# Optimization experiments

Measured on AMD Instinct MI355X. Metric: run time of the kernel, lower is better.

Reference implementation:

```python
import jax, jax.numpy as jnp
import numpy as np

# Static config matching init_kwargs
DG = 8          # deformable groups
KH, KW = 3, 3
STRIDE, PAD, DIL = 1, 1, 1


def setup_inputs() -> dict:
    key = jax.random.key(0)
    k1, k2, k3, k4 = jax.random.split(key, 4)
    B, C, H, W = 4, 128, 128, 128
    Cout = 128
    K = KH * KW
    x = jax.random.normal(k1, (B, C, H, W), dtype=jnp.float32)
    offset = jax.random.normal(k2, (B, 2 * DG * K, H, W), dtype=jnp.float32)
    mask = jax.random.uniform(k3, (B, DG * K, H, W), dtype=jnp.float32)
    stdv = 1.0 / np.sqrt(C * KH * KW)
    weight = jax.random.uniform(k4, (Cout, C, KH, KW), dtype=jnp.float32,
                                minval=-stdv, maxval=stdv)
    bias = jnp.zeros((Cout,), dtype=jnp.float32)
    return {"x": x, "offset": offset, "mask": mask, "weight": weight, "bias": bias}


def _deform_conv2d(x, offset, mask, weight, bias):
    B, C, H, W = x.shape
    Cout = weight.shape[0]
    K = KH * KW
    Ho = (H + 2 * PAD - DIL * (KH - 1) - 1) // STRIDE + 1
    Wo = (W + 2 * PAD - DIL * (KW - 1) - 1) // STRIDE + 1
    Cg = C // DG

    # offsets: channel layout [dg, k, (dy, dx)]
    off = offset.reshape(B, DG, K, 2, Ho, Wo)
    dy, dx = off[:, :, :, 0], off[:, :, :, 1]          # [B, DG, K, Ho, Wo]
    m = mask.reshape(B, DG, K, Ho, Wo)

    ky, kx = jnp.meshgrid(jnp.arange(KH), jnp.arange(KW), indexing='ij')
    ky, kx = ky.reshape(K), kx.reshape(K)
    # base sampling grid per kernel tap: [K, Ho] / [K, Wo]
    py = (jnp.arange(Ho) * STRIDE - PAD)[None, :] + (ky * DIL)[:, None]
    px = (jnp.arange(Wo) * STRIDE - PAD)[None, :] + (kx * DIL)[:, None]

    sy = dy + py[None, None, :, :, None].astype(dy.dtype)  # [B, DG, K, Ho, Wo]
    sx = dx + px[None, None, :, None, :].astype(dx.dtype)

    y0f = jnp.floor(sy); x0f = jnp.floor(sx)
    ly = sy - y0f; lx = sx - x0f
    y0 = y0f.astype(jnp.int32); x0 = x0f.astype(jnp.int32)

    x_g = x.reshape(B, DG, Cg, H * W)

    def gather(iy, ix):
        valid = ((iy >= 0) & (iy < H) & (ix >= 0) & (ix < W)).astype(x.dtype)
        idx = jnp.clip(iy, 0, H - 1) * W + jnp.clip(ix, 0, W - 1)
        flat = idx.reshape(B, DG, 1, K * Ho * Wo)
        v = jnp.take_along_axis(x_g, flat, axis=3).reshape(B, DG, Cg, K, Ho, Wo)
        return v * valid[:, :, None]

    w00 = ((1 - ly) * (1 - lx))[:, :, None]
    w01 = ((1 - ly) * lx)[:, :, None]
    w10 = (ly * (1 - lx))[:, :, None]
    w11 = (ly * lx)[:, :, None]

    val = (gather(y0, x0) * w00 + gather(y0, x0 + 1) * w01 +
           gather(y0 + 1, x0) * w10 + gather(y0 + 1, x0 + 1) * w11)
    val = val * m[:, :, None]                         # modulation
    sampled = val.reshape(B, C, K, Ho, Wo)

    w = weight.reshape(Cout, C, K)
    out = jnp.einsum('bckhw,ock->bohw', sampled, w)
    return out + bias[None, :, None, None]


def reference(x, offset, mask, weight, bias):
    return _deform_conv2d(x, offset, mask, weight, bias)
```

## Files before the change

kernel.cpp:

```cpp
#include <hip/hip_runtime.h>
#include <hip/hip_fp16.h>


#define NB    4
#define NC    128
#define NH    128
#define NW    128
#define NCOUT 128
#define NDG   8
#define NCG   16
#define NK    9
#define NCK   1152
#define NHW   16384
#define GK    160
#define ROWP  168
#define WROW  1280

typedef __attribute__((ext_vector_type(4))) float f32x4;
typedef _Float16 half8 __attribute__((ext_vector_type(8)));

union C16 { uint4 u[2]; __half2 h[8]; };

__device__ __forceinline__ unsigned pk2h(float a, float b) {
  return (unsigned)__half_as_ushort(__float2half_rn(a)) |
         ((unsigned)__half_as_ushort(__float2half_rn(b)) << 16);
}

__global__ __launch_bounds__(256)
void prep(const float* __restrict__ x, const float* __restrict__ w,
          ushort* __restrict__ xt, ushort* __restrict__ wf) {
  __shared__ __align__(16) unsigned LDSU[1024 * 9];
  const int tid = threadIdx.x;

  if (blockIdx.x < 128) {
    const int o = blockIdx.x;
    float* WL = (float*)LDSU;
    const float4* src = (const float4*)(w + o * NCK);
    for (int i = tid; i < NCK / 4; i += 256) ((float4*)WL)[i] = src[i];
    __syncthreads();
    unsigned* dst = (unsigned*)wf + o * (WROW / 2);
    for (int t = tid; t < WROW / 2; t += 256) {
      const int g = t / 80, r = t - g * 80;
      unsigned v = 0;
      if (r < 72) {
        const int k = r >> 3;
        const int c = g * NCG + (r & 7) * 2;
        v = pk2h(WL[c * NK + k], WL[(c + 1) * NK + k]);
      }
      dst[t] = v;
    }
  } else {
    const int blk  = blockIdx.x - 128;
    const int slab = blk >> 4;
    const int hw0  = (blk & 15) * 1024;
    const float* xb = x + (size_t)slab * NCG * NHW + hw0;
#pragma unroll
    for (int cp = 0; cp < 8; ++cp) {
#pragma unroll
      for (int i = 0; i < 4; ++i) {
        const int hw = tid + 256 * i;
        LDSU[hw * 9 + cp] =
            pk2h(xb[(2 * cp) * NHW + hw], xb[(2 * cp + 1) * NHW + hw]);
      }
    }
    __syncthreads();
    uint4* dst = (uint4*)(xt + ((size_t)slab * NHW + hw0) * NCG);
#pragma unroll
    for (int j = 0; j < 8; ++j) {
      const int lin = tid + 256 * j;
      const int hw = lin >> 1, q = lin & 1;
      uint4 v;
      v.x = LDSU[hw * 9 + q * 4 + 0];
      v.y = LDSU[hw * 9 + q * 4 + 1];
      v.z = LDSU[hw * 9 + q * 4 + 2];
      v.w = LDSU[hw * 9 + q * 4 + 3];
      dst[lin] = v;
    }
  }
}

__device__ __forceinline__ void sample_one(
    int p, int k, int g, int b, int ho, int wo0,
    float dy, float dx, float mm,
    const ushort* __restrict__ xt, ushort* __restrict__ S) {
  const int ky = k / 3, kx = k - ky * 3;

  const float sy = dy + (float)(ho - 1 + ky);
  const float sx = dx + (float)(wo0 + p - 1 + kx);
  const float y0f = floorf(sy), x0f = floorf(sx);
  const float ly = sy - y0f, lx = sx - x0f;
  const int y0 = (int)y0f, x0 = (int)x0f;
  const int y1 = y0 + 1,  x1 = x0 + 1;
  const float hy = 1.f - ly, hx = 1.f - lx;

  float w00 = hy * hx * mm, w01 = hy * lx * mm;
  float w10 = ly * hx * mm, w11 = ly * lx * mm;
  if (y0 < 0 || y0 >= NH) { w00 = 0.f; w01 = 0.f; }
  if (y1 < 0 || y1 >= NH) { w10 = 0.f; w11 = 0.f; }
  if (x0 < 0 || x0 >= NW) { w00 = 0.f; w10 = 0.f; }
  if (x1 < 0 || x1 >= NW) { w01 = 0.f; w11 = 0.f; }

  const int yc0 = min(max(y0, 0), NH - 1);
  const int yc1 = min(max(y1, 0), NH - 1);
  const int xc0 = min(max(x0, 0), NW - 1);
  const int xc1 = min(max(x1, 0), NW - 1);

  const ushort* xg = xt + (size_t)(b * NDG + g) * NHW * NCG;
  const uint4* q00 = (const uint4*)(xg + (yc0 * NW + xc0) * NCG);
  const uint4* q01 = (const uint4*)(xg + (yc0 * NW + xc1) * NCG);
  const uint4* q10 = (const uint4*)(xg + (yc1 * NW + xc0) * NCG);
  const uint4* q11 = (const uint4*)(xg + (yc1 * NW + xc1) * NCG);

  C16 v00, v01, v10, v11, r;
  v00.u[0] = q00[0]; v00.u[1] = q00[1];
  v01.u[0] = q01[0]; v01.u[1] = q01[1];
  v10.u[0] = q10[0]; v10.u[1] = q10[1];
  v11.u[0] = q11[0]; v11.u[1] = q11[1];

  const __half2 W00 = __float2half2_rn(w00);
  const __half2 W01 = __float2half2_rn(w01);
  const __half2 W10 = __float2half2_rn(w10);
  const __half2 W11 = __float2half2_rn(w11);
#pragma unroll
  for (int i = 0; i < 8; ++i) {
    __half2 a = __hmul2(v00.h[i], W00);
    a = __hfma2(v01.h[i], W01, a);
    a = __hfma2(v10.h[i], W10, a);
    a = __hfma2(v11.h[i], W11, a);
    r.h[i] = a;
  }
  ushort* dp = &S[p * ROWP + k * 16];
  *(uint4*)dp = r.u[0];
  *((uint4*)dp + 1) = r.u[1];
}

__global__ __launch_bounds__(256, 4)
void dcn_main(const float* __restrict__ off,
              const float* __restrict__ msk,
              const ushort* __restrict__ xt,
              const ushort* __restrict__ wf,
              const float* __restrict__ bias,
              float* __restrict__ out) {
  __shared__ __align__(16) ushort S[64 * ROWP];

  const int tid  = threadIdx.x;
  const int blk0 = blockIdx.x;
  const int blk  = (blk0 & 7) * 128 + (blk0 >> 3);
  const int b    = blk >> 8;
  const int ho   = (blk >> 1) & 127;
  const int wo0  = (blk & 1) * 64;

  const int lane = tid & 63;
  const int wv   = tid >> 6;
  const int l15  = lane & 15;
  const int kq   = lane >> 4;

  const float* offB = off + (size_t)b * 144 * NHW + ho * NW + wo0;
  const float* mskB = msk + (size_t)b * 72  * NHW + ho * NW + wo0;

  for (int i = tid; i < 64 * 8; i += 256) {
    ((unsigned*)S)[(i >> 3) * (ROWP / 2) + 72 + (i & 7)] = 0;
  }

  f32x4 acc[4][2];
#pragma unroll
  for (int m = 0; m < 4; ++m) {
    acc[m][0] = {0.f, 0.f, 0.f, 0.f};
    acc[m][1] = {0.f, 0.f, 0.f, 0.f};
  }

  const int p0 = tid & 63;
  const int k0 = tid >> 6;
  const int k1 = k0 + 4;

  float dy0, dx0, mm0, dy1, dx1, mm1, dy2 = 0.f, dx2 = 0.f, mm2 = 0.f;
  {
    const int gka = k0, gkb = k1;
    dy0 = offB[(gka * 2) * NHW + p0];
    dx0 = offB[(gka * 2 + 1) * NHW + p0];
    mm0 = mskB[gka * NHW + p0];
    dy1 = offB[(gkb * 2) * NHW + p0];
    dx1 = offB[(gkb * 2 + 1) * NHW + p0];
    mm1 = mskB[gkb * NHW + p0];
    if (tid < 64) {
      dy2 = offB[16 * NHW + p0];
      dx2 = offB[17 * NHW + p0];
      mm2 = mskB[8 * NHW + p0];
    }
  }

  for (int g = 0; g < 8; ++g) {
    if (g) __syncthreads();

    sample_one(p0, k0, g, b, ho, wo0, dy0, dx0, mm0, xt, S);
    sample_one(p0, k1, g, b, ho, wo0, dy1, dx1, mm1, xt, S);
    if (tid < 64) sample_one(p0, 8, g, b, ho, wo0, dy2, dx2, mm2, xt, S);

    if (g < 7) {
      const int gka = (g + 1) * 9 + k0, gkb = (g + 1) * 9 + k1;
      dy0 = offB[(gka * 2) * NHW + p0];
      dx0 = offB[(gka * 2 + 1) * NHW + p0];
      mm0 = mskB[gka * NHW + p0];
      dy1 = offB[(gkb * 2) * NHW + p0];
      dx1 = offB[(gkb * 2 + 1) * NHW + p0];
      mm1 = mskB[gkb * NHW + p0];
      if (tid < 64) {
        const int gkc = (g + 1) * 9 + 8;
        dy2 = offB[(gkc * 2) * NHW + p0];
        dx2 = offB[(gkc * 2 + 1) * NHW + p0];
        mm2 = mskB[gkc * NHW + p0];
      }
    }
    __syncthreads();

    const ushort* bw0 = wf + (size_t)(wv * 32 + l15) * WROW + g * GK + kq * 8;
    const ushort* bw1 = bw0 + 16 * WROW;
    const ushort* sa  = &S[l15 * ROWP + kq * 8];
#pragma unroll
    for (int ks = 0; ks < 5; ++ks) {
      const half8 bf0 = *(const half8*)(bw0 + ks * 32);
      const half8 bf1 = *(const half8*)(bw1 + ks * 32);
#pragma unroll
      for (int m = 0; m < 4; ++m) {
        const half8 a = *(const half8*)(sa + m * 16 * ROWP + ks * 32);
        acc[m][0] = __builtin_amdgcn_mfma_f32_16x16x32_f16(a, bf0, acc[m][0], 0, 0, 0);
        acc[m][1] = __builtin_amdgcn_mfma_f32_16x16x32_f16(a, bf1, acc[m][1], 0, 0, 0);
      }
    }
  }

#pragma unroll
  for (int j = 0; j < 2; ++j) {
    const int c0 = wv * 32 + j * 16 + l15;
    const float bs = bias[c0];
    float* op = out + (size_t)(b * NCOUT + c0) * NHW + ho * NW + wo0 + kq * 4;
#pragma unroll
    for (int m = 0; m < 4; ++m) {
      float4 r = {acc[m][j][0] + bs, acc[m][j][1] + bs,
                  acc[m][j][2] + bs, acc[m][j][3] + bs};
      *(float4*)(op + m * 16) = r;
    }
  }
}

extern "C" void kernel_launch(void* const* d_in, const int* in_sizes, int n_in,
                              void* d_out, int out_size, void* d_ws, size_t ws_size,
                              hipStream_t stream) {
  const float* x    = (const float*)d_in[0];
  const float* off  = (const float*)d_in[1];
  const float* msk  = (const float*)d_in[2];
  const float* wgt  = (const float*)d_in[3];
  const float* bias = (const float*)d_in[4];
  float* out = (float*)d_out;

  ushort* xt = (ushort*)d_ws;
  ushort* wf = xt + (size_t)NB * NDG * NHW * NCG;

  hipLaunchKernelGGL(prep, dim3(640), dim3(256), 0, stream, x, wgt, xt, wf);
  hipLaunchKernelGGL(dcn_main, dim3(1024), dim3(256), 0, stream,
                     off, msk, xt, wf, bias, out);
}
```

Before: 209.3 us.

## Process full output rows per 512-thread block with MFMA-friendly weight layout

Each block now covers a whole 128-pixel output row with 8 waves split over pixel halves and output-channel quarters, where before it covered half a row with 4 waves. The weight buffer is repacked so each lane's B-fragment loads coalesce across output channels, and those weight fragments are prefetched into registers before the sampling phase. This halves the block count and hides weight-load latency behind the gather, at the cost of more registers per thread and a larger LDS tile.

```diff
diff --git a/kernel.cpp b/kernel.cpp
--- a/kernel.cpp
+++ b/kernel.cpp
@@ -14,7 +14,6 @@
 #define NHW   16384
 #define GK    160
 #define ROWP  168
-#define WROW  1280
 
 typedef __attribute__((ext_vector_type(4))) float f32x4;
 typedef _Float16 half8 __attribute__((ext_vector_type(8)));
@@ -38,8 +37,8 @@
     const float4* src = (const float4*)(w + o * NCK);
     for (int i = tid; i < NCK / 4; i += 256) ((float4*)WL)[i] = src[i];
     __syncthreads();
-    unsigned* dst = (unsigned*)wf + o * (WROW / 2);
-    for (int t = tid; t < WROW / 2; t += 256) {
+    unsigned* dstw = (unsigned*)wf;
+    for (int t = tid; t < 640; t += 256) {
       const int g = t / 80, r = t - g * 80;
       unsigned v = 0;
       if (r < 72) {
@@ -47,7 +46,10 @@
         const int c = g * NCG + (r & 7) * 2;
         v = pk2h(WL[c * NK + k], WL[(c + 1) * NK + k]);
       }
-      dst[t] = v;
+      const int ks = r >> 4;
+      const int kq = (r >> 2) & 3;
+      const int ep = r & 3;
+      dstw[((((g * 5 + ks) * 4 + kq) * 128) + o) * 4 + ep] = v;
     }
   } else {
     const int blk  = blockIdx.x - 128;
@@ -80,13 +82,12 @@
 }
 
 __device__ __forceinline__ void sample_one(
-    int p, int k, int g, int b, int ho, int wo0,
-    float dy, float dx, float mm,
+    int p, int k, int g, int b, int ho, float dy, float dx, float mm,
     const ushort* __restrict__ xt, ushort* __restrict__ S) {
   const int ky = k / 3, kx = k - ky * 3;
 
   const float sy = dy + (float)(ho - 1 + ky);
-  const float sx = dx + (float)(wo0 + p - 1 + kx);
+  const float sx = dx + (float)(p - 1 + kx);
   const float y0f = floorf(sy), x0f = floorf(sx);
   const float ly = sy - y0f, lx = sx - x0f;
   const int y0 = (int)y0f, x0 = (int)x0f;
@@ -134,31 +135,33 @@
   *((uint4*)dp + 1) = r.u[1];
 }
 
-__global__ __launch_bounds__(256, 4)
+__global__ __launch_bounds__(512, 4)
 void dcn_main(const float* __restrict__ off,
               const float* __restrict__ msk,
               const ushort* __restrict__ xt,
               const ushort* __restrict__ wf,
               const float* __restrict__ bias,
               float* __restrict__ out) {
-  __shared__ __align__(16) ushort S[64 * ROWP];
+  __shared__ __align__(16) ushort S[128 * ROWP];
 
   const int tid  = threadIdx.x;
   const int blk0 = blockIdx.x;
-  const int blk  = (blk0 & 7) * 128 + (blk0 >> 3);
-  const int b    = blk >> 8;
-  const int ho   = (blk >> 1) & 127;
-  const int wo0  = (blk & 1) * 64;
+  const int blk  = (blk0 & 7) * 64 + (blk0 >> 3);
+  const int b    = blk >> 7;
+  const int ho   = blk & 127;
 
   const int lane = tid & 63;
   const int wv   = tid >> 6;
   const int l15  = lane & 15;
   const int kq   = lane >> 4;
-
-  const float* offB = off + (size_t)b * 144 * NHW + ho * NW + wo0;
-  const float* mskB = msk + (size_t)b * 72  * NHW + ho * NW + wo0;
-
-  for (int i = tid; i < 64 * 8; i += 256) {
+  const int mh   = (wv & 1) * 4;
+  const int nb   = wv >> 1;
+  const int cbase = nb * 32 + l15;
+
+  const float* offB = off + (size_t)b * 144 * NHW + ho * NW;
+  const float* mskB = msk + (size_t)b * 72  * NHW + ho * NW;
+
+  for (int i = tid; i < 128 * 8; i += 512) {
     ((unsigned*)S)[(i >> 3) * (ROWP / 2) + 72 + (i & 7)] = 0;
   }
 
@@ -169,20 +172,19 @@
     acc[m][1] = {0.f, 0.f, 0.f, 0.f};
   }
 
-  const int p0 = tid & 63;
-  const int k0 = tid >> 6;
+  const int p0 = tid & 127;
+  const int k0 = tid >> 7;
   const int k1 = k0 + 4;
 
   float dy0, dx0, mm0, dy1, dx1, mm1, dy2 = 0.f, dx2 = 0.f, mm2 = 0.f;
   {
-    const int gka = k0, gkb = k1;
-    dy0 = offB[(gka * 2) * NHW + p0];
-    dx0 = offB[(gka * 2 + 1) * NHW + p0];
-    mm0 = mskB[gka * NHW + p0];
-    dy1 = offB[(gkb * 2) * NHW + p0];
-    dx1 = offB[(gkb * 2 + 1) * NHW + p0];
-    mm1 = mskB[gkb * NHW + p0];
-    if (tid < 64) {
+    dy0 = offB[(k0 * 2) * NHW + p0];
+    dx0 = offB[(k0 * 2 + 1) * NHW + p0];
+    mm0 = mskB[k0 * NHW + p0];
+    dy1 = offB[(k1 * 2) * NHW + p0];
+    dx1 = offB[(k1 * 2 + 1) * NHW + p0];
+    mm1 = mskB[k1 * NHW + p0];
+    if (tid < 128) {
       dy2 = offB[16 * NHW + p0];
       dx2 = offB[17 * NHW + p0];
       mm2 = mskB[8 * NHW + p0];
@@ -192,9 +194,19 @@
   for (int g = 0; g < 8; ++g) {
     if (g) __syncthreads();
 
-    sample_one(p0, k0, g, b, ho, wo0, dy0, dx0, mm0, xt, S);
-    sample_one(p0, k1, g, b, ho, wo0, dy1, dx1, mm1, xt, S);
-    if (tid < 64) sample_one(p0, 8, g, b, ho, wo0, dy2, dx2, mm2, xt, S);
+    half8 bf0[5], bf1[5];
+    {
+      const ushort* wb = wf + ((size_t)(g * 20 + kq) * 128 + cbase) * 8;
+#pragma unroll
+      for (int ks = 0; ks < 5; ++ks) {
+        bf0[ks] = *(const half8*)(wb + ks * 4096);
+        bf1[ks] = *(const half8*)(wb + ks * 4096 + 128);
+      }
+    }
+
+    sample_one(p0, k0, g, b, ho, dy0, dx0, mm0, xt, S);
+    sample_one(p0, k1, g, b, ho, dy1, dx1, mm1, xt, S);
+    if (tid < 128) sample_one(p0, 8, g, b, ho, dy2, dx2, mm2, xt, S);
 
     if (g < 7) {
       const int gka = (g + 1) * 9 + k0, gkb = (g + 1) * 9 + k1;
@@ -204,7 +216,7 @@
       dy1 = offB[(gkb * 2) * NHW + p0];
       dx1 = offB[(gkb * 2 + 1) * NHW + p0];
       mm1 = mskB[gkb * NHW + p0];
-      if (tid < 64) {
+      if (tid < 128) {
         const int gkc = (g + 1) * 9 + 8;
         dy2 = offB[(gkc * 2) * NHW + p0];
         dx2 = offB[(gkc * 2 + 1) * NHW + p0];
@@ -213,32 +225,28 @@
     }
     __syncthreads();
 
-    const ushort* bw0 = wf + (size_t)(wv * 32 + l15) * WROW + g * GK + kq * 8;
-    const ushort* bw1 = bw0 + 16 * WROW;
-    const ushort* sa  = &S[l15 * ROWP + kq * 8];
+    const ushort* sa = &S[l15 * ROWP + kq * 8];
 #pragma unroll
     for (int ks = 0; ks < 5; ++ks) {
-      const half8 bf0 = *(const half8*)(bw0 + ks * 32);
-      const half8 bf1 = *(const half8*)(bw1 + ks * 32);
 #pragma unroll
       for (int m = 0; m < 4; ++m) {
-        const half8 a = *(const half8*)(sa + m * 16 * ROWP + ks * 32);
-        acc[m][0] = __builtin_amdgcn_mfma_f32_16x16x32_f16(a, bf0, acc[m][0], 0, 0, 0);
-        acc[m][1] = __builtin_amdgcn_mfma_f32_16x16x32_f16(a, bf1, acc[m][1], 0, 0, 0);
+        const half8 a = *(const half8*)(sa + (mh + m) * 16 * ROWP + ks * 32);
+        acc[m][0] = __builtin_amdgcn_mfma_f32_16x16x32_f16(a, bf0[ks], acc[m][0], 0, 0, 0);
+        acc[m][1] = __builtin_amdgcn_mfma_f32_16x16x32_f16(a, bf1[ks], acc[m][1], 0, 0, 0);
       }
     }
   }
 
 #pragma unroll
   for (int j = 0; j < 2; ++j) {
-    const int c0 = wv * 32 + j * 16 + l15;
+    const int c0 = nb * 32 + j * 16 + l15;
     const float bs = bias[c0];
-    float* op = out + (size_t)(b * NCOUT + c0) * NHW + ho * NW + wo0 + kq * 4;
+    float* op = out + (size_t)(b * NCOUT + c0) * NHW + ho * NW + kq * 4;
 #pragma unroll
     for (int m = 0; m < 4; ++m) {
       float4 r = {acc[m][j][0] + bs, acc[m][j][1] + bs,
                   acc[m][j][2] + bs, acc[m][j][3] + bs};
-      *(float4*)(op + m * 16) = r;
+      *(float4*)(op + (mh + m) * 16) = r;
     }
   }
 }
@@ -257,6 +265,6 @@
   ushort* wf = xt + (size_t)NB * NDG * NHW * NCG;
 
   hipLaunchKernelGGL(prep, dim3(640), dim3(256), 0, stream, x, wgt, xt, wf);
-  hipLaunchKernelGGL(dcn_main, dim3(1024), dim3(256), 0, stream,
+  hipLaunchKernelGGL(dcn_main, dim3(512), dim3(512), 0, stream,
                      off, msk, xt, wf, bias, out);
 }
```

Result: slower. 221.4 us (+5.8%).
